# Performance work log

Hardware: AMD Instinct MI355X
Metric: run time of the kernel (lower is better)

## Reference

```python
import math
import jax, jax.numpy as jnp
import numpy as np

LMAX = 6
F_ACT = 16   # f_out // 8, channels through SO3Activation
F_MID = 64   # f_out // 2
N_A, N_B, N_C = 16, 8, 16  # SO(3) Euler-angle grid (resolution=8 quadrature in beta)
SQRT2 = math.sqrt(2.0)     # normalize2mom factor for relu

# ---- Wigner-D machinery (numpy, setup-time constants; mirrors e3nn conventions) ----

def _su2_generators(j):
    m = np.arange(-j, j)
    raising = np.diag(-np.sqrt(j * (j + 1) - m * (m + 1)), k=-1).astype(complex)
    m = np.arange(-j + 1, j + 1)
    lowering = np.diag(np.sqrt(j * (j + 1) - m * (m - 1)), k=1).astype(complex)
    m = np.arange(-j, j + 1)
    return np.stack([0.5 * (raising + lowering), np.diag(1j * m), -0.5j * (raising - lowering)])

def _q_real(l):
    q = np.zeros((2 * l + 1, 2 * l + 1), dtype=complex)
    for m in range(-l, 0):
        q[l + m, l + abs(m)] = 2 ** -0.5
        q[l + m, l - abs(m)] = -1j * 2 ** -0.5
    q[l, l] = 1
    for m in range(1, l + 1):
        q[l + m, l + abs(m)] = (-1) ** m * 2 ** -0.5
        q[l + m, l - abs(m)] = 1j * (-1) ** m * 2 ** -0.5
    return (-1j) ** l * q

def _so3_generators(l):
    X = _su2_generators(l)
    Q = _q_real(l)
    return np.real(np.einsum('ij,njk,kl->nil', np.conj(Q.T), X, Q))

def _expm(A):
    w, V = np.linalg.eig(A.astype(complex))
    return np.real((V * np.exp(w)) @ np.linalg.inv(V))

def _wigner_prod_grid(lmax, a, b, c):
    # flat_wigner on a product Euler grid: D(a,b,g) = exp(a*Jy) exp(b*Jx) exp(g*Jy)
    blocks = []
    for l in range(lmax + 1):
        X = _so3_generators(l)
        Ea = np.stack([_expm(t * X[1]) for t in a])
        Eb = np.stack([_expm(t * X[0]) for t in b])
        Ec = np.stack([_expm(t * X[1]) for t in c])
        D = np.einsum('amn,bnp,cpq->abcmq', Ea, Eb, Ec)
        blocks.append((2 * l + 1) ** 0.5 * D.reshape(len(a) * len(b) * len(c), -1))
    return np.concatenate(blocks, -1)

def _flat_wigner_pts(lmax, a, b, c):
    blocks = []
    for l in range(lmax + 1):
        X = _so3_generators(l)
        D = np.stack([_expm(ai * X[1]) @ _expm(bi * X[0]) @ _expm(ci * X[1]) for ai, bi, ci in zip(a, b, c)])
        blocks.append((2 * l + 1) ** 0.5 * D.reshape(len(a), -1))
    return np.concatenate(blocks, -1)

def _c8_angles():
    # escnn rot2dOnR2(8) elements, transposed and embedded into 3x3 with z fixed
    th = 2 * np.pi * np.arange(8) / 8
    M = np.zeros((8, 3, 3))
    M[:, 0, 0] = np.cos(th); M[:, 0, 1] = np.sin(th)
    M[:, 1, 0] = -np.sin(th); M[:, 1, 1] = np.cos(th)
    M[:, 2, 2] = 1.0
    x = M @ np.array([0.0, 1.0, 0.0])
    b = np.arccos(np.clip(x[:, 1], -1, 1))
    a = np.arctan2(x[:, 0], x[:, 2])
    def my(t): c, s = np.cos(t), np.sin(t); return np.array([[c, 0, s], [0, 1, 0], [-s, 0, c]])
    def mx(t): c, s = np.cos(t), np.sin(t); return np.array([[1, 0, 0], [0, c, -s], [0, s, c]])
    g = np.array([np.arctan2(R[0, 2], R[0, 0]) for R in [(my(a[i]) @ mx(b[i])).T @ M[i] for i in range(8)]])
    return a, b, g

# ---- precomputed constants ----
_A = 2 * np.pi * np.arange(N_A) / N_A
_XB, _WB = np.polynomial.legendre.leggauss(N_B)
_B = np.arccos(_XB)
_C = 2 * np.pi * np.arange(N_C) / N_C
D_IN = jnp.asarray(_wigner_prod_grid(1, _A, _B, _C), jnp.float32)                 # (G, 10)
_QW = np.broadcast_to((_WB / 2.0)[None, :, None] / (N_A * N_C), (N_A, N_B, N_C)).reshape(-1)
D_OUTW = jnp.asarray(_wigner_prod_grid(LMAX, _A, _B, _C) * _QW[:, None], jnp.float32)  # (G, 455), quadrature folded in
C8W = jnp.asarray(_flat_wigner_pts(LMAX, *_c8_angles()), jnp.float32)             # (8, 455)


def setup_inputs() -> dict:
    key = jax.random.key(0)
    ks = jax.random.split(key, 16)
    inp = {
        'x': jax.random.normal(ks[0], (16, 32, 128, 455), jnp.float32),
        'trajectory': jax.random.normal(ks[1], (16, 32, 10), jnp.float32),
        'w1_l0': jax.random.normal(ks[2], (1, F_ACT, 1, 1), jnp.float32),
        'w1_l1': jax.random.normal(ks[3], (1, F_ACT, 3, 3), jnp.float32),
    }
    for l in range(LMAX + 1):
        d = 2 * l + 1
        inp[f'w2_l{l}'] = jax.random.normal(ks[4 + l], (F_ACT, F_MID, d, d), jnp.float32)
    return inp


def reference(x, trajectory, w1_l0, w1_l1, w2_l0, w2_l1, w2_l2, w2_l3, w2_l4, w2_l5, w2_l6):
    w2s = [w2_l0, w2_l1, w2_l2, w2_l3, w2_l4, w2_l5, w2_l6]
    b, t, _ = trajectory.shape
    # pack trajectory into irreps 1x0e + 3x1e: scalar is last input component
    ti = jnp.concatenate([trajectory[..., 9:10], trajectory[..., :9]], axis=-1)  # (b,t,10)
    # proj_1 (o3.Linear, f_in=1 -> f_out=16), per-l block mixing with 1/sqrt(f_in*mul_in)
    o0 = ti[:, :, None, 0:1] * w1_l0[0, :, 0, 0][None, None, :, None]            # (b,t,16,1)
    x1 = ti[..., 1:10].reshape(b, t, 3, 3)                                       # (mul=3, m=3)
    o1 = jnp.einsum('btum,guw->btgwm', x1, w1_l1[0]) * (3.0 ** -0.5)             # (b,t,16,3,3)
    feat = jnp.concatenate([o0, o1.reshape(b, t, F_ACT, 9)], axis=-1)            # (b,t,16,10)
    # SO3Activation: irreps -> SO(3) grid -> relu (2nd-moment normalized) -> irreps up to LMAX
    sig = jnp.einsum('btci,gi->btcg', feat, D_IN)                                # (b,t,16,G)
    sig = jax.nn.relu(sig) * SQRT2
    feat = jnp.einsum('btcg,gi->btci', sig, D_OUTW)                              # (b,t,16,455)
    # proj_2 (o3.Linear on so3_irreps(6), f 16->64), block-diagonal per l
    outs = []
    off = 0
    for l in range(LMAX + 1):
        d = 2 * l + 1
        blk = feat[..., off:off + d * d].reshape(b, t, F_ACT, d, d)
        o = jnp.einsum('btfum,fguw->btgwm', blk, w2s[l]) * ((F_ACT * d) ** -0.5)
        outs.append(o.reshape(b, t, F_MID, d * d))
        off += d * d
    traj_out = jnp.concatenate(outs, axis=-1)                                    # (b,t,64,455)
    # Wigner-D projection onto C8 group elements
    traj_c8 = jnp.einsum('btcj,ij->btci', traj_out, C8W)                         # (b,t,64,8)
    x_c8 = jnp.einsum('bhcj,ij->bhci', x, C8W)                                   # (b,h,128,8)
    return x_c8, traj_c8
```

## Files before the change

kernel.cpp:

```cpp
#include <hip/hip_runtime.h>
#include <hip/hip_bf16.h>
#include <math.h>


typedef __attribute__((ext_vector_type(8))) short bf16x8;
typedef __attribute__((ext_vector_type(4))) float f32x4;
typedef __attribute__((ext_vector_type(16))) float f32x16;

__device__ const int c_offs[8] = {0, 1, 10, 35, 84, 165, 286, 455};

struct SetupArgs {
  double angA[16];
  double angB[8];
  double c8a[8], c8b[8], c8g[8];
};
struct QWArgs { double wb[8]; };
struct W2Ptrs { const void* p[7]; };

__device__ __forceinline__ float bf2f(unsigned short u) {
  union { unsigned int i; float f; } v; v.i = ((unsigned int)u) << 16; return v.f;
}
__device__ __forceinline__ unsigned short f2bf(float f) {
  union { float f; unsigned int i; } v; v.f = f;
  unsigned int r = v.i + 0x7fffu + ((v.i >> 16) & 1u);
  return (unsigned short)(r >> 16);
}
__device__ __forceinline__ float in_val(const void* p, size_t i, int isf) {
  return isf ? ((const float*)p)[i] : bf2f(((const unsigned short*)p)[i]);
}
__device__ __forceinline__ void gl_lds16(const void* g, void* lds) {
  __builtin_amdgcn_global_load_lds(
      (const __attribute__((address_space(1))) unsigned int*)g,
      (__attribute__((address_space(3))) unsigned int*)lds, 16, 0, 0);
}
__device__ __forceinline__ void wait_bar() {
  asm volatile("s_waitcnt vmcnt(0)\n\ts_barrier" ::: "memory");
}

__global__ __launch_bounds__(192) void k_exps(SetupArgs args, double* exps,
                                              const void* x, int* flag) {
  __shared__ double Qr[169], Qi[169], Bm[169], R[169];
  __shared__ double coefA[13], coefB[13], rowsum[13];
  __shared__ double snorm;
  __shared__ int cnt;
  int tid = threadIdx.x;

  if (blockIdx.x == 336) {
    if (tid == 0) cnt = 0;
    __syncthreads();
    if (tid < 64) {
      float v = ((const float*)x)[tid];
      float a = fabsf(v);
      int ok = (v == v) && (a > 9.0949470e-13f) && (a < 1.0995116e12f);
      atomicAdd(&cnt, ok);
    }
    __syncthreads();
    if (tid == 0) *flag = (cnt >= 32) ? 1 : 0;
    return;
  }

  int l = blockIdx.x / 48, item = blockIdx.x % 48;
  int e = tid;
  bool val = (e < 169);
  int r = e / 13, c = e % 13;

  if (val) { Qr[e] = 0.0; Qi[e] = 0.0; }
  __syncthreads();
  if (tid == 0) {
    const double is2 = 0.70710678118654752440;
    for (int m = -l; m <= l; m++) {
      int rr = l + m;
      if (m < 0) {
        Qr[rr * 13 + (l - m)] = is2;
        Qi[rr * 13 + (l + m)] = -is2;
      } else if (m == 0) {
        Qr[l * 13 + l] = 1.0;
      } else {
        double s = (m & 1) ? -1.0 : 1.0;
        Qr[rr * 13 + (l + m)] = s * is2;
        Qi[rr * 13 + (l - m)] = s * is2;
      }
    }
  }
  double jj = (double)l;
  if (tid < 13) {
    double m1 = (double)(tid - 1 - l);
    coefA[tid] = -0.5 * sqrt(fmax(jj * (jj + 1.0) - m1 * (m1 + 1.0), 0.0));
    double m2 = (double)(tid + 1 - l);
    coefB[tid] = 0.5 * sqrt(fmax(jj * (jj + 1.0) - m2 * (m2 - 1.0), 0.0));
  }
  __syncthreads();
  {
    int lm = l & 3;
    double pr = (lm == 0) ? 1.0 : (lm == 2 ? -1.0 : 0.0);
    double pi = (lm == 1) ? -1.0 : (lm == 3 ? 1.0 : 0.0);
    if (val) {
      double qr = Qr[e], qi = Qi[e];
      Qr[e] = qr * pr - qi * pi;
      Qi[e] = qr * pi + qi * pr;
    }
  }
  __syncthreads();

  double t; int axis;
  if (item < 16)      { t = args.angA[item];      axis = 1; }
  else if (item < 24) { t = args.angB[item - 16]; axis = 0; }
  else if (item < 32) { t = args.c8a[item - 24];  axis = 1; }
  else if (item < 40) { t = args.c8b[item - 32];  axis = 0; }
  else                { t = args.c8g[item - 40];  axis = 1; }

  if (val) {
    double accr = 0.0;
    if (axis == 1) {
#pragma unroll
      for (int p = 0; p < 13; p++) {
        double mp = (double)(p - l);
        double ar = Qr[p * 13 + r], ai = -Qi[p * 13 + r];
        double br = Qr[p * 13 + c], bi = Qi[p * 13 + c];
        accr += -mp * (ar * bi + ai * br);
      }
    } else {
#pragma unroll
      for (int p = 0; p < 13; p++) {
        double xr = 0.0, xi = 0.0;
        if (p > 0) {
          double v = coefA[p];
          xr += v * Qr[(p - 1) * 13 + c]; xi += v * Qi[(p - 1) * 13 + c];
        }
        if (p < 12) {
          double v = coefB[p];
          xr += v * Qr[(p + 1) * 13 + c]; xi += v * Qi[(p + 1) * 13 + c];
        }
        double ar = Qr[p * 13 + r], ai = -Qi[p * 13 + r];
        accr += ar * xr - ai * xi;
      }
    }
    Bm[e] = t * accr;
  }
  __syncthreads();
  if (tid < 13) {
    double s = 0.0;
#pragma unroll
    for (int cc = 0; cc < 13; cc++) s += fabs(Bm[tid * 13 + cc]);
    rowsum[tid] = s;
  }
  __syncthreads();
  if (tid == 0) {
    double mx = 0.0;
#pragma unroll
    for (int rr = 0; rr < 13; rr++) mx = fmax(mx, rowsum[rr]);
    int s = 0;
    while (mx > 0.5 && s < 48) { mx *= 0.5; s++; }
    snorm = (double)s;
  }
  __syncthreads();
  int sq = (int)snorm;
  double sc = 1.0;
  for (int i = 0; i < sq; i++) sc *= 0.5;
  if (val) {
    double b = Bm[e] * sc;
    Bm[e] = b;
    R[e] = b / 16.0 + ((r == c) ? 1.0 : 0.0);
  }
  __syncthreads();
  for (int k = 15; k >= 1; k--) {
    double acc = 0.0;
    if (val) {
#pragma unroll
      for (int p = 0; p < 13; p++) acc += Bm[r * 13 + p] * R[p * 13 + c];
    }
    __syncthreads();
    if (val) R[e] = acc / (double)k + ((r == c) ? 1.0 : 0.0);
    __syncthreads();
  }
  for (int i = 0; i < sq; i++) {
    double acc = 0.0;
    if (val) {
#pragma unroll
      for (int p = 0; p < 13; p++) acc += R[r * 13 + p] * R[p * 13 + c];
    }
    __syncthreads();
    if (val) R[e] = acc;
    __syncthreads();
  }
  double* out = exps + (size_t)blockIdx.x * 169;
  if (val) out[e] = R[e];
}

__global__ __launch_bounds__(192) void k_assemble(const double* exps, QWArgs qw,
                                                  unsigned short* dwt, float* dint,
                                                  float* c8w,
                                                  const void* traj, const void* w1l0,
                                                  const void* w1l1, float* feat,
                                                  const int* flag) {
  __shared__ double Ea[169], Eb[169], Ec[169], T1[169];
  int tid = threadIdx.x;
  int bx = blockIdx.x;

  if (bx >= 3640) {
    int isf = __builtin_amdgcn_readfirstlane(flag[0]);
    int idx = (bx - 3640) * 192 + tid;
    if (idx >= 512 * 160) return;
    int bt = idx / 160, rem = idx % 160;
    int c = rem / 10, i = rem % 10;
    float v;
    if (i == 0) {
      v = in_val(traj, bt * 10 + 9, isf) * in_val(w1l0, c, isf);
    } else {
      int ii = i - 1, w = ii / 3, m = ii % 3;
      float acc = 0.0f;
      for (int u = 0; u < 3; u++)
        acc += in_val(traj, bt * 10 + 3 * u + m, isf) *
               in_val(w1l1, c * 9 + u * 3 + w, isf);
      v = acc * 0.57735026918962576f;
    }
    feat[idx] = v;
    return;
  }

  int e = tid;
  bool valp = (e < 169);
  int r = e / 13, c = e % 13;

  if (bx >= 3584) {
    int idx = bx - 3584;
    int l = idx / 8, ci = idx % 8;
    int d = 2 * l + 1;
    const double* pa = exps + (size_t)(l * 48 + 24 + ci) * 169;
    const double* pb = exps + (size_t)(l * 48 + 32 + ci) * 169;
    const double* pc = exps + (size_t)(l * 48 + 40 + ci) * 169;
    if (valp) { Ea[e] = pa[e]; Eb[e] = pb[e]; Ec[e] = pc[e]; }
    __syncthreads();
    if (valp) {
      double acc = 0.0;
#pragma unroll
      for (int p = 0; p < 13; p++) acc += Ea[r * 13 + p] * Eb[p * 13 + c];
      T1[e] = acc;
    }
    __syncthreads();
    double scale = sqrt((double)(2 * l + 1));
    if (valp) {
      double acc = 0.0;
#pragma unroll
      for (int p = 0; p < 13; p++) acc += T1[r * 13 + p] * Ec[p * 13 + c];
      if (r < d && c < d)
        c8w[ci * 512 + c_offs[l] + r * d + c] = (float)(scale * acc);
    }
    if (l == 0) {
      for (int jz = 455 + tid; jz < 512; jz += 192)
        c8w[ci * 512 + jz] = 0.0f;
    }
    return;
  }

  int l = bx / 512, rem = bx % 512;
  int a = rem >> 5, b = (rem >> 2) & 7, cg = rem & 3;
  int d = 2 * l + 1;
  const double* pa = exps + (size_t)(l * 48 + a) * 169;
  const double* pb = exps + (size_t)(l * 48 + 16 + b) * 169;
  if (valp) { Ea[e] = pa[e]; Eb[e] = pb[e]; }
  __syncthreads();
  if (valp) {
    double acc = 0.0;
#pragma unroll
    for (int p = 0; p < 13; p++) acc += Ea[r * 13 + p] * Eb[p * 13 + c];
    T1[e] = acc;
  }
  double scale = sqrt((double)(2 * l + 1));
  double qwv = qw.wb[b] * (1.0 / 512.0);
  bool inblk = valp && (r < d) && (c < d);
  int j = inblk ? (c_offs[l] + r * d + c) : 0;
  const double* ctab = exps + (size_t)(l * 48) * 169;
  for (int cc = cg * 4; cc < cg * 4 + 4; cc++) {
    __syncthreads();
    if (valp) Ec[e] = ctab[(size_t)cc * 169 + e];
    __syncthreads();
    int g = a * 128 + b * 16 + cc;
    if (valp) {
      double acc = 0.0;
#pragma unroll
      for (int p = 0; p < 13; p++) acc += T1[r * 13 + p] * Ec[p * 13 + c];
      if (inblk) {
        dwt[(size_t)j * 2048 + g] = f2bf((float)(scale * acc * qwv));
        if (l == 1) dint[(size_t)(1 + r * 3 + c) * 2048 + g] = (float)(scale * acc);
        if (l == 0 && e == 0) dint[g] = (float)(scale * acc);
      }
    }
    if (l == 0) {
      for (int jz = 455 + tid; jz < 512; jz += 192)
        dwt[(size_t)jz * 2048 + g] = 0;
    }
  }
}

__global__ __launch_bounds__(256) void k_sig(const float* feat, const float* dint,
                                             unsigned short* sig) {
  int bi = blockIdx.x >> 3;
  int g = ((blockIdx.x & 7) << 8) + threadIdx.x;
  float din[10];
#pragma unroll
  for (int i = 0; i < 10; i++) din[i] = dint[(size_t)i * 2048 + g];
  const float* fr = feat + bi * 160;
  for (int cc = 0; cc < 16; cc++) {
    float acc = 0.0f;
#pragma unroll
    for (int i = 0; i < 10; i++) acc += fr[cc * 10 + i] * din[i];
    acc = fmaxf(acc, 0.0f) * 1.41421356237309505f;
    sig[(size_t)(bi * 16 + cc) * 2048 + g] = f2bf(acc);
  }
}

__global__ __launch_bounds__(256) void k_ebuild(W2Ptrs w2, const float* c8w,
                                                unsigned short* et, const int* flag) {
  int isf = __builtin_amdgcn_readfirstlane(flag[0]);
  int base = (blockIdx.x * 256 + threadIdx.x) * 4;
  int n = base >> 13;
  int rest = base & 8191;
  int f = rest >> 9, jj0 = rest & 511;
  int g = n >> 3, i = n & 7;
  unsigned short ov[4];
#pragma unroll
  for (int s = 0; s < 4; s++) {
    int jj = jj0 + s;
    if (jj >= 455) { ov[s] = 0; continue; }
    int l    = (jj >= 1) + (jj >= 10) + (jj >= 35) + (jj >= 84) +
               (jj >= 165) + (jj >= 286);
    int offs = jj >= 286 ? 286 : jj >= 165 ? 165 : jj >= 84 ? 84 :
               jj >= 35 ? 35 : jj >= 10 ? 10 : jj >= 1 ? 1 : 0;
    int mg   = jj >= 286 ? 20165 : jj >= 165 ? 23832 : jj >= 84 ? 29128 :
               jj >= 35 ? 37450 : jj >= 10 ? 52429 : jj >= 1 ? 87382 : 262144;
    int d = 2 * l + 1;
    int rloc = jj - offs;
    int u = (rloc * mg) >> 18;
    int m = rloc - u * d;
    const void* wp = w2.p[0];
    wp = (l >= 1) ? w2.p[1] : wp;
    wp = (l >= 2) ? w2.p[2] : wp;
    wp = (l >= 3) ? w2.p[3] : wp;
    wp = (l >= 4) ? w2.p[4] : wp;
    wp = (l >= 5) ? w2.p[5] : wp;
    wp = (l >= 6) ? w2.p[6] : wp;
    float acc = 0.0f;
    for (int w = 0; w < d; w++) {
      float wv = in_val(wp, ((size_t)(f * 64 + g) * d + u) * d + w, isf);
      acc += wv * c8w[i * 512 + offs + w * d + m];
    }
    acc *= rsqrtf((float)(16 * d));
    ov[s] = f2bf(acc);
  }
  *(ushort4*)&et[(size_t)n * 8192 + f * 512 + jj0] =
      make_ushort4(ov[0], ov[1], ov[2], ov[3]);
}

__global__ __launch_bounds__(256) void k_gemm2(const unsigned short* A,
                                               const unsigned short* B,
                                               unsigned short* C) {
  __shared__ __align__(16) unsigned short As[2][128 * 64];
  __shared__ __align__(16) unsigned short Bs[2][64 * 64];
  int tid = threadIdx.x;
  int lane = tid & 63, wid = tid >> 6;
  int xcd = blockIdx.x & 7, bi = blockIdx.x >> 3;
  int mt = xcd * 8 + (bi >> 3), nt = bi & 7;
  int m0 = mt * 128, n0 = nt * 64;
  int wm = wid >> 1, wn = wid & 1;
  f32x16 acc[2];
#pragma unroll
  for (int t = 0; t < 2; t++)
#pragma unroll
    for (int r = 0; r < 16; r++) acc[t][r] = 0.0f;

  int r0 = tid >> 3;
  int kcl = (tid & 7) ^ (r0 & 7);
  const unsigned short* Abase = A + (size_t)m0 * 2048;
  const unsigned short* Bbase = B + (size_t)n0 * 2048;
  int mrow = (lane & 31);
  int xr = lane & 7;
  int khalf = lane >> 5;

  auto STAGE = [&](int buf, int kt) {
    int k0 = kt * 64;
#pragma unroll
    for (int i = 0; i < 4; i++)
      gl_lds16(Abase + (size_t)(i * 32 + r0) * 2048 + k0 + kcl * 8,
               &As[buf][i * 2048 + wid * 512]);
#pragma unroll
    for (int i = 0; i < 2; i++)
      gl_lds16(Bbase + (size_t)(i * 32 + r0) * 2048 + k0 + kcl * 8,
               &Bs[buf][i * 2048 + wid * 512]);
  };

  STAGE(0, 0);
  wait_bar();
  int cur = 0;
  for (int kt = 0; kt < 32; kt++) {
    if (kt < 31) STAGE(cur ^ 1, kt + 1);
#pragma unroll
    for (int q = 0; q < 4; q++) {
      int qc = q * 2 + khalf;
      bf16x8 bv = *(const bf16x8*)&Bs[cur][(wn * 32 + mrow) * 64 + (qc ^ xr) * 8];
#pragma unroll
      for (int t = 0; t < 2; t++) {
        bf16x8 av = *(const bf16x8*)&As[cur][(wm * 64 + t * 32 + mrow) * 64 + (qc ^ xr) * 8];
        acc[t] = __builtin_amdgcn_mfma_f32_32x32x16_bf16(av, bv, acc[t], 0, 0, 0);
      }
    }
    if (kt < 31) { wait_bar(); cur ^= 1; }
  }
  int col = n0 + wn * 32 + (lane & 31);
#pragma unroll
  for (int t = 0; t < 2; t++)
#pragma unroll
    for (int r = 0; r < 16; r++) {
      int row = m0 + wm * 64 + t * 32 + (r & 3) + 8 * (r >> 2) + 4 * (lane >> 5);
      C[(size_t)row * 512 + col] = f2bf(acc[t][r]);
    }
}

__global__ __launch_bounds__(256) void k_gemm3(const unsigned short* A,
                                               const unsigned short* B, float* Cp) {
  __shared__ __align__(16) unsigned short As[2][64 * 32];
  __shared__ __align__(16) unsigned short Bs[2][128 * 32];
  int tid = threadIdx.x, lane = tid & 63, wid = tid >> 6;
  int mt = blockIdx.x >> 5, kc = (blockIdx.x >> 2) & 7, nt = blockIdx.x & 3;
  int m0 = mt * 64, n0 = nt * 128;
  int wm = wid >> 1, wn = wid & 1;
  f32x4 acc[2][4];
#pragma unroll
  for (int a = 0; a < 2; a++)
#pragma unroll
    for (int b = 0; b < 4; b++) acc[a][b] = (f32x4){0.f, 0.f, 0.f, 0.f};
  int ar = tid >> 2, ak = (tid & 3) * 8;
  const unsigned short* Abase = A + (size_t)m0 * 8192 + kc * 1024;
  const unsigned short* Bbase = B + (size_t)n0 * 8192 + kc * 1024;
  int row = lane & 15, kq = (lane >> 4) * 8;

  auto STAGE = [&](int buf, int kt) {
    int k0 = kt * 32;
    gl_lds16(Abase + (size_t)ar * 8192 + k0 + ak, &As[buf][wid * 512]);
    gl_lds16(Bbase + (size_t)ar * 8192 + k0 + ak, &Bs[buf][wid * 512]);
    gl_lds16(Bbase + (size_t)(ar + 64) * 8192 + k0 + ak, &Bs[buf][2048 + wid * 512]);
  };

  STAGE(0, 0);
  wait_bar();
  int cur = 0;
  for (int kt = 0; kt < 32; kt++) {
    if (kt < 31) STAGE(cur ^ 1, kt + 1);
    bf16x8 af[2], bfr[4];
#pragma unroll
    for (int im = 0; im < 2; im++)
      af[im] = *(const bf16x8*)&As[cur][(wm * 32 + im * 16 + row) * 32 + kq];
#pragma unroll
    for (int in = 0; in < 4; in++)
      bfr[in] = *(const bf16x8*)&Bs[cur][(wn * 64 + in * 16 + row) * 32 + kq];
#pragma unroll
    for (int im = 0; im < 2; im++)
#pragma unroll
      for (int in = 0; in < 4; in++)
        acc[im][in] = __builtin_amdgcn_mfma_f32_16x16x32_bf16(af[im], bfr[in],
                                                              acc[im][in], 0, 0, 0);
    if (kt < 31) { wait_bar(); cur ^= 1; }
  }
  int col = lane & 15, rq = (lane >> 4) * 4;
  float* out = Cp + (size_t)kc * 262144;
#pragma unroll
  for (int im = 0; im < 2; im++)
#pragma unroll
    for (int in = 0; in < 4; in++)
#pragma unroll
      for (int r = 0; r < 4; r++) {
        int rr = m0 + wm * 32 + im * 16 + rq + r;
        int cc = n0 + wn * 64 + in * 16 + col;
        out[(size_t)rr * 512 + cc] = acc[im][in][r];
      }
}

__global__ __launch_bounds__(256) void k_xc8r(const void* x, const float* c8w,
                                              const float* Cp, void* dout,
                                              const int* flag) {
  int tid = threadIdx.x, lane = tid & 63, wid = tid >> 6;
  int isf = __builtin_amdgcn_readfirstlane(flag[0]);

  if (blockIdx.x >= 2048) {
    int idx = (blockIdx.x - 2048) * 256 + tid;
    const float4* c = (const float4*)Cp;
    float s0 = 0.f, s1 = 0.f, s2 = 0.f, s3 = 0.f;
#pragma unroll
    for (int p = 0; p < 8; p++) {
      float4 v = c[idx + p * 65536];
      s0 += v.x; s1 += v.y; s2 += v.z; s3 += v.w;
    }
    size_t base = 524288 + (size_t)idx * 4;
    if (isf) {
      float4 o; o.x = s0; o.y = s1; o.z = s2; o.w = s3;
      *(float4*)((float*)dout + base) = o;
    } else {
      unsigned int p0 = (unsigned int)f2bf(s0) | ((unsigned int)f2bf(s1) << 16);
      unsigned int p1 = (unsigned int)f2bf(s2) | ((unsigned int)f2bf(s3) << 16);
      uint2 pk; pk.x = p0; pk.y = p1;
      *(uint2*)((unsigned short*)dout + base) = pk;
    }
    return;
  }

  int gw = blockIdx.x * 4 + wid;
  float cw[8][8];
#pragma unroll
  for (int t = 0; t < 8; t++)
#pragma unroll
    for (int i = 0; i < 8; i++)
      cw[t][i] = c8w[i * 512 + t * 64 + lane];
  const float* xf = (const float*)x;
  const unsigned short* xh = (const unsigned short*)x;
  for (int r = gw * 8; r < gw * 8 + 8; r++) {
    float acc[8];
#pragma unroll
    for (int i = 0; i < 8; i++) acc[i] = 0.0f;
    if (isf) {
      const float* xr = xf + (size_t)r * 455;
#pragma unroll
      for (int t = 0; t < 8; t++) {
        int j = t * 64 + lane;
        float xv = (j < 455) ? xr[j] : 0.0f;
#pragma unroll
        for (int i = 0; i < 8; i++) acc[i] += xv * cw[t][i];
      }
    } else {
      const unsigned short* xr = xh + (size_t)r * 455;
#pragma unroll
      for (int t = 0; t < 8; t++) {
        int j = t * 64 + lane;
        float xv = (j < 455) ? bf2f(xr[j]) : 0.0f;
#pragma unroll
        for (int i = 0; i < 8; i++) acc[i] += xv * cw[t][i];
      }
    }
#pragma unroll
    for (int off = 1; off <= 4; off <<= 1)
#pragma unroll
      for (int i = 0; i < 8; i++) acc[i] += __shfl_xor(acc[i], off);
    int lg = lane & 7;
    float v = acc[0];
    v = (lg == 1) ? acc[1] : v;
    v = (lg == 2) ? acc[2] : v;
    v = (lg == 3) ? acc[3] : v;
    v = (lg == 4) ? acc[4] : v;
    v = (lg == 5) ? acc[5] : v;
    v = (lg == 6) ? acc[6] : v;
    v = (lg == 7) ? acc[7] : v;
    v += __shfl_xor(v, 8);
    v += __shfl_xor(v, 16);
    v += __shfl_xor(v, 32);
    if (lane < 8) {
      if (isf) ((float*)dout)[(size_t)r * 8 + lane] = v;
      else     ((unsigned short*)dout)[(size_t)r * 8 + lane] = f2bf(v);
    }
  }
}

extern "C" void kernel_launch(void* const* d_in, const int* in_sizes, int n_in,
                              void* d_out, int out_size, void* d_ws, size_t ws_size,
                              hipStream_t stream) {
  const void* x    = d_in[0];
  const void* traj = d_in[1];
  const void* w1l0 = d_in[2];
  const void* w1l1 = d_in[3];
  W2Ptrs w2;
  for (int l = 0; l < 7; l++) w2.p[l] = d_in[4 + l];

  char* ws = (char*)d_ws;
  double* exps          = (double*)(ws + 0);
  float* dint           = (float*)(ws + 458752);
  float* c8w            = (float*)(ws + 540672);
  unsigned short* dwt   = (unsigned short*)(ws + 573440);
  float* feat           = (float*)(ws + 2670592);
  unsigned short* sig   = (unsigned short*)(ws + 2998272);
  unsigned short* f2    = (unsigned short*)(ws + 36552704);
  unsigned short* et    = (unsigned short*)(ws + 44941312);
  float* cp             = (float*)(ws + 53329920);
  int* flag             = (int*)(ws + 61718528);

  SetupArgs sa; QWArgs qa;
  for (int i = 0; i < 16; i++) sa.angA[i] = 2.0 * M_PI * (double)i / 16.0;
  static const double XB[8] = {
    -0.9602898564975363, -0.7966664774136267, -0.5255324099163290,
    -0.1834346424956498,  0.1834346424956498,  0.5255324099163290,
     0.7966664774136267,  0.9602898564975363};
  static const double WBv[8] = {
     0.1012285362903763, 0.2223810344533745, 0.3137066458778873,
     0.3626837833783620, 0.3626837833783620, 0.3137066458778873,
     0.2223810344533745, 0.1012285362903763};
  for (int i = 0; i < 8; i++) { sa.angB[i] = acos(XB[i]); qa.wb[i] = WBv[i]; }
  for (int i = 0; i < 8; i++) {
    double th = 2.0 * M_PI * (double)i / 8.0;
    double Mm[3][3] = {{cos(th), sin(th), 0.0},
                       {-sin(th), cos(th), 0.0},
                       {0.0, 0.0, 1.0}};
    double x0 = Mm[0][1], x1 = Mm[1][1], x2 = Mm[2][1];
    double bb = acos(fmax(-1.0, fmin(1.0, x1)));
    double aa = atan2(x0, x2);
    double ca_ = cos(aa), sa_ = sin(aa), cb_ = cos(bb), sb_ = sin(bb);
    double MY[3][3] = {{ca_, 0, sa_}, {0, 1, 0}, {-sa_, 0, ca_}};
    double MX[3][3] = {{1, 0, 0}, {0, cb_, -sb_}, {0, sb_, cb_}};
    double P1[3][3], Rr[3][3];
    for (int r = 0; r < 3; r++)
      for (int c = 0; c < 3; c++) {
        double s = 0.0;
        for (int k = 0; k < 3; k++) s += MY[r][k] * MX[k][c];
        P1[r][c] = s;
      }
    for (int r = 0; r < 3; r++)
      for (int c = 0; c < 3; c++) {
        double s = 0.0;
        for (int k = 0; k < 3; k++) s += P1[k][r] * Mm[k][c];
        Rr[r][c] = s;
      }
    double gg = atan2(Rr[0][2], Rr[0][0]);
    sa.c8a[i] = aa; sa.c8b[i] = bb; sa.c8g[i] = gg;
  }

  k_exps<<<337, 192, 0, stream>>>(sa, exps, x, flag);
  k_assemble<<<4067, 192, 0, stream>>>(exps, qa, dwt, dint, c8w,
                                       traj, w1l0, w1l1, feat, flag);
  k_sig<<<4096, 256, 0, stream>>>(feat, dint, sig);
  k_ebuild<<<4096, 256, 0, stream>>>(w2, c8w, et, flag);
  k_gemm2<<<512, 256, 0, stream>>>(sig, dwt, f2);
  k_gemm3<<<256, 256, 0, stream>>>(f2, et, cp);
  k_xc8r<<<2304, 256, 0, stream>>>(x, c8w, cp, d_out, flag);
}
```

Baseline: 328.2 us.

## Vectorize assemble stores, merge sig/ebuild kernels, triple-buffer both GEMMs

k_assemble now has each block handle all 16 gamma angles, so the dwt and dint writes become 16-byte vector stores instead of scattered 2-byte and 4-byte ones. The launch grid shrinks to match. k_sig and k_ebuild are merged into one k_post launch to remove a kernel launch. Both GEMMs move from double to triple buffering with partial vmcnt waits, so loads run two stages ahead. k_gemm3 also switches to 64x64 tiles with twice as many blocks, which adds parallelism but raises redundant A-tile reloads.

```diff
diff --git a/kernel.cpp b/kernel.cpp
--- a/kernel.cpp
+++ b/kernel.cpp
@@ -32,9 +32,6 @@
   __builtin_amdgcn_global_load_lds(
       (const __attribute__((address_space(1))) unsigned int*)g,
       (__attribute__((address_space(3))) unsigned int*)lds, 16, 0, 0);
-}
-__device__ __forceinline__ void wait_bar() {
-  asm volatile("s_waitcnt vmcnt(0)\n\ts_barrier" ::: "memory");
 }
 
 __global__ __launch_bounds__(192) void k_exps(SetupArgs args, double* exps,
@@ -197,9 +194,9 @@
   int tid = threadIdx.x;
   int bx = blockIdx.x;
 
-  if (bx >= 3640) {
+  if (bx >= 952) {
     int isf = __builtin_amdgcn_readfirstlane(flag[0]);
-    int idx = (bx - 3640) * 192 + tid;
+    int idx = (bx - 952) * 192 + tid;
     if (idx >= 512 * 160) return;
     int bt = idx / 160, rem = idx % 160;
     int c = rem / 10, i = rem % 10;
@@ -222,8 +219,8 @@
   bool valp = (e < 169);
   int r = e / 13, c = e % 13;
 
-  if (bx >= 3584) {
-    int idx = bx - 3584;
+  if (bx >= 896) {
+    int idx = bx - 896;
     int l = idx / 8, ci = idx % 8;
     int d = 2 * l + 1;
     const double* pa = exps + (size_t)(l * 48 + 24 + ci) * 169;
@@ -253,8 +250,8 @@
     return;
   }
 
-  int l = bx / 512, rem = bx % 512;
-  int a = rem >> 5, b = (rem >> 2) & 7, cg = rem & 3;
+  int l = bx >> 7, rem = bx & 127;
+  int a = rem >> 3, b = rem & 7;
   int d = 2 * l + 1;
   const double* pa = exps + (size_t)(l * 48 + a) * 169;
   const double* pb = exps + (size_t)(l * 48 + 16 + b) * 169;
@@ -270,50 +267,74 @@
   double qwv = qw.wb[b] * (1.0 / 512.0);
   bool inblk = valp && (r < d) && (c < d);
   int j = inblk ? (c_offs[l] + r * d + c) : 0;
+  int g0 = a * 128 + b * 16;
   const double* ctab = exps + (size_t)(l * 48) * 169;
-  for (int cc = cg * 4; cc < cg * 4 + 4; cc++) {
+  unsigned int ow[8];
+  float dv[16];
+#pragma unroll
+  for (int cc = 0; cc < 16; cc++) {
     __syncthreads();
     if (valp) Ec[e] = ctab[(size_t)cc * 169 + e];
     __syncthreads();
-    int g = a * 128 + b * 16 + cc;
+    double acc = 0.0;
     if (valp) {
-      double acc = 0.0;
 #pragma unroll
       for (int p = 0; p < 13; p++) acc += T1[r * 13 + p] * Ec[p * 13 + c];
-      if (inblk) {
-        dwt[(size_t)j * 2048 + g] = f2bf((float)(scale * acc * qwv));
-        if (l == 1) dint[(size_t)(1 + r * 3 + c) * 2048 + g] = (float)(scale * acc);
-        if (l == 0 && e == 0) dint[g] = (float)(scale * acc);
-      }
+    }
+    unsigned int hv = (unsigned int)f2bf((float)(scale * acc * qwv));
+    if ((cc & 1) == 0) ow[cc >> 1] = hv;
+    else               ow[cc >> 1] |= hv << 16;
+    dv[cc] = (float)(scale * acc);
+  }
+  if (inblk) {
+    unsigned short* wp = &dwt[(size_t)j * 2048 + g0];
+    *(uint4*)&wp[0] = make_uint4(ow[0], ow[1], ow[2], ow[3]);
+    *(uint4*)&wp[8] = make_uint4(ow[4], ow[5], ow[6], ow[7]);
+    if (l == 1) {
+      float* dp = &dint[(size_t)(1 + r * 3 + c) * 2048 + g0];
+      *(float4*)&dp[0]  = make_float4(dv[0],  dv[1],  dv[2],  dv[3]);
+      *(float4*)&dp[4]  = make_float4(dv[4],  dv[5],  dv[6],  dv[7]);
+      *(float4*)&dp[8]  = make_float4(dv[8],  dv[9],  dv[10], dv[11]);
+      *(float4*)&dp[12] = make_float4(dv[12], dv[13], dv[14], dv[15]);
     }
     if (l == 0) {
-      for (int jz = 455 + tid; jz < 512; jz += 192)
-        dwt[(size_t)jz * 2048 + g] = 0;
-    }
-  }
-}
-
-__global__ __launch_bounds__(256) void k_sig(const float* feat, const float* dint,
-                                             unsigned short* sig) {
-  int bi = blockIdx.x >> 3;
-  int g = ((blockIdx.x & 7) << 8) + threadIdx.x;
-  float din[10];
-#pragma unroll
-  for (int i = 0; i < 10; i++) din[i] = dint[(size_t)i * 2048 + g];
-  const float* fr = feat + bi * 160;
-  for (int cc = 0; cc < 16; cc++) {
-    float acc = 0.0f;
-#pragma unroll
-    for (int i = 0; i < 10; i++) acc += fr[cc * 10 + i] * din[i];
-    acc = fmaxf(acc, 0.0f) * 1.41421356237309505f;
-    sig[(size_t)(bi * 16 + cc) * 2048 + g] = f2bf(acc);
-  }
-}
-
-__global__ __launch_bounds__(256) void k_ebuild(W2Ptrs w2, const float* c8w,
-                                                unsigned short* et, const int* flag) {
+      float* dp = &dint[g0];
+      *(float4*)&dp[0]  = make_float4(dv[0],  dv[1],  dv[2],  dv[3]);
+      *(float4*)&dp[4]  = make_float4(dv[4],  dv[5],  dv[6],  dv[7]);
+      *(float4*)&dp[8]  = make_float4(dv[8],  dv[9],  dv[10], dv[11]);
+      *(float4*)&dp[12] = make_float4(dv[12], dv[13], dv[14], dv[15]);
+    }
+  }
+  if (l == 0 && tid < 57) {
+    unsigned short* zp = &dwt[(size_t)(455 + tid) * 2048 + g0];
+    *(uint4*)&zp[0] = make_uint4(0, 0, 0, 0);
+    *(uint4*)&zp[8] = make_uint4(0, 0, 0, 0);
+  }
+}
+
+__global__ __launch_bounds__(256) void k_post(const float* feat, const float* dint,
+                                              unsigned short* sig, W2Ptrs w2,
+                                              const float* c8w, unsigned short* et,
+                                              const int* flag) {
+  int bx = blockIdx.x;
+  if (bx < 4096) {
+    int bi = bx >> 3;
+    int g = ((bx & 7) << 8) + threadIdx.x;
+    float din[10];
+#pragma unroll
+    for (int i = 0; i < 10; i++) din[i] = dint[(size_t)i * 2048 + g];
+    const float* fr = feat + bi * 160;
+    for (int cc = 0; cc < 16; cc++) {
+      float acc = 0.0f;
+#pragma unroll
+      for (int i = 0; i < 10; i++) acc += fr[cc * 10 + i] * din[i];
+      acc = fmaxf(acc, 0.0f) * 1.41421356237309505f;
+      sig[(size_t)(bi * 16 + cc) * 2048 + g] = f2bf(acc);
+    }
+    return;
+  }
   int isf = __builtin_amdgcn_readfirstlane(flag[0]);
-  int base = (blockIdx.x * 256 + threadIdx.x) * 4;
+  int base = ((bx - 4096) * 256 + threadIdx.x) * 4;
   int n = base >> 13;
   int rest = base & 8191;
   int f = rest >> 9, jj0 = rest & 511;
@@ -355,8 +376,8 @@
 __global__ __launch_bounds__(256) void k_gemm2(const unsigned short* A,
                                                const unsigned short* B,
                                                unsigned short* C) {
-  __shared__ __align__(16) unsigned short As[2][128 * 64];
-  __shared__ __align__(16) unsigned short Bs[2][64 * 64];
+  __shared__ __align__(16) unsigned short As[3][128 * 64];
+  __shared__ __align__(16) unsigned short Bs[3][64 * 64];
   int tid = threadIdx.x;
   int lane = tid & 63, wid = tid >> 6;
   int xcd = blockIdx.x & 7, bi = blockIdx.x >> 3;
@@ -390,21 +411,27 @@
   };
 
   STAGE(0, 0);
-  wait_bar();
-  int cur = 0;
+  STAGE(1, 1);
+  int cb = 0;
   for (int kt = 0; kt < 32; kt++) {
-    if (kt < 31) STAGE(cur ^ 1, kt + 1);
+    if (kt < 31) asm volatile("s_waitcnt vmcnt(6)" ::: "memory");
+    else         asm volatile("s_waitcnt vmcnt(0)" ::: "memory");
+    __builtin_amdgcn_s_barrier();
+    __builtin_amdgcn_sched_barrier(0);
+    const unsigned short* Ab = As[cb];
+    const unsigned short* Bb = Bs[cb];
 #pragma unroll
     for (int q = 0; q < 4; q++) {
       int qc = q * 2 + khalf;
-      bf16x8 bv = *(const bf16x8*)&Bs[cur][(wn * 32 + mrow) * 64 + (qc ^ xr) * 8];
+      bf16x8 bv = *(const bf16x8*)&Bb[(wn * 32 + mrow) * 64 + (qc ^ xr) * 8];
 #pragma unroll
       for (int t = 0; t < 2; t++) {
-        bf16x8 av = *(const bf16x8*)&As[cur][(wm * 64 + t * 32 + mrow) * 64 + (qc ^ xr) * 8];
+        bf16x8 av = *(const bf16x8*)&Ab[(wm * 64 + t * 32 + mrow) * 64 + (qc ^ xr) * 8];
         acc[t] = __builtin_amdgcn_mfma_f32_32x32x16_bf16(av, bv, acc[t], 0, 0, 0);
       }
     }
-    if (kt < 31) { wait_bar(); cur ^= 1; }
+    if (kt < 30) STAGE(cb == 0 ? 2 : cb - 1, kt + 2);
+    cb = (cb == 2) ? 0 : cb + 1;
   }
   int col = n0 + wn * 32 + (lane & 31);
 #pragma unroll
@@ -418,17 +445,17 @@
 
 __global__ __launch_bounds__(256) void k_gemm3(const unsigned short* A,
                                                const unsigned short* B, float* Cp) {
-  __shared__ __align__(16) unsigned short As[2][64 * 32];
-  __shared__ __align__(16) unsigned short Bs[2][128 * 32];
+  __shared__ __align__(16) unsigned short As[3][64 * 32];
+  __shared__ __align__(16) unsigned short Bs[3][64 * 32];
   int tid = threadIdx.x, lane = tid & 63, wid = tid >> 6;
-  int mt = blockIdx.x >> 5, kc = (blockIdx.x >> 2) & 7, nt = blockIdx.x & 3;
-  int m0 = mt * 64, n0 = nt * 128;
+  int kc = blockIdx.x >> 6, mt = (blockIdx.x >> 3) & 7, nt = blockIdx.x & 7;
+  int m0 = mt * 64, n0 = nt * 64;
   int wm = wid >> 1, wn = wid & 1;
-  f32x4 acc[2][4];
+  f32x4 acc[2][2];
 #pragma unroll
   for (int a = 0; a < 2; a++)
 #pragma unroll
-    for (int b = 0; b < 4; b++) acc[a][b] = (f32x4){0.f, 0.f, 0.f, 0.f};
+    for (int b = 0; b < 2; b++) acc[a][b] = (f32x4){0.f, 0.f, 0.f, 0.f};
   int ar = tid >> 2, ak = (tid & 3) * 8;
   const unsigned short* Abase = A + (size_t)m0 * 8192 + kc * 1024;
   const unsigned short* Bbase = B + (size_t)n0 * 8192 + kc * 1024;
@@ -438,39 +465,42 @@
     int k0 = kt * 32;
     gl_lds16(Abase + (size_t)ar * 8192 + k0 + ak, &As[buf][wid * 512]);
     gl_lds16(Bbase + (size_t)ar * 8192 + k0 + ak, &Bs[buf][wid * 512]);
-    gl_lds16(Bbase + (size_t)(ar + 64) * 8192 + k0 + ak, &Bs[buf][2048 + wid * 512]);
   };
 
   STAGE(0, 0);
-  wait_bar();
-  int cur = 0;
+  STAGE(1, 1);
+  int cb = 0;
   for (int kt = 0; kt < 32; kt++) {
-    if (kt < 31) STAGE(cur ^ 1, kt + 1);
-    bf16x8 af[2], bfr[4];
+    if (kt < 31) asm volatile("s_waitcnt vmcnt(2)" ::: "memory");
+    else         asm volatile("s_waitcnt vmcnt(0)" ::: "memory");
+    __builtin_amdgcn_s_barrier();
+    __builtin_amdgcn_sched_barrier(0);
+    bf16x8 af[2], bfr[2];
 #pragma unroll
     for (int im = 0; im < 2; im++)
-      af[im] = *(const bf16x8*)&As[cur][(wm * 32 + im * 16 + row) * 32 + kq];
-#pragma unroll
-    for (int in = 0; in < 4; in++)
-      bfr[in] = *(const bf16x8*)&Bs[cur][(wn * 64 + in * 16 + row) * 32 + kq];
+      af[im] = *(const bf16x8*)&As[cb][(wm * 32 + im * 16 + row) * 32 + kq];
+#pragma unroll
+    for (int in = 0; in < 2; in++)
+      bfr[in] = *(const bf16x8*)&Bs[cb][(wn * 32 + in * 16 + row) * 32 + kq];
 #pragma unroll
     for (int im = 0; im < 2; im++)
 #pragma unroll
-      for (int in = 0; in < 4; in++)
+      for (int in = 0; in < 2; in++)
         acc[im][in] = __builtin_amdgcn_mfma_f32_16x16x32_bf16(af[im], bfr[in],
                                                               acc[im][in], 0, 0, 0);
-    if (kt < 31) { wait_bar(); cur ^= 1; }
+    if (kt < 30) STAGE(cb == 0 ? 2 : cb - 1, kt + 2);
+    cb = (cb == 2) ? 0 : cb + 1;
   }
   int col = lane & 15, rq = (lane >> 4) * 4;
   float* out = Cp + (size_t)kc * 262144;
 #pragma unroll
   for (int im = 0; im < 2; im++)
 #pragma unroll
-    for (int in = 0; in < 4; in++)
+    for (int in = 0; in < 2; in++)
 #pragma unroll
       for (int r = 0; r < 4; r++) {
         int rr = m0 + wm * 32 + im * 16 + rq + r;
-        int cc = n0 + wn * 64 + in * 16 + col;
+        int cc = n0 + wn * 32 + in * 16 + col;
         out[(size_t)rr * 512 + cc] = acc[im][in][r];
       }
 }
@@ -620,11 +650,10 @@
   }
 
   k_exps<<<337, 192, 0, stream>>>(sa, exps, x, flag);
-  k_assemble<<<4067, 192, 0, stream>>>(exps, qa, dwt, dint, c8w,
+  k_assemble<<<1379, 192, 0, stream>>>(exps, qa, dwt, dint, c8w,
                                        traj, w1l0, w1l1, feat, flag);
-  k_sig<<<4096, 256, 0, stream>>>(feat, dint, sig);
-  k_ebuild<<<4096, 256, 0, stream>>>(w2, c8w, et, flag);
+  k_post<<<8192, 256, 0, stream>>>(feat, dint, sig, w2, c8w, et, flag);
   k_gemm2<<<512, 256, 0, stream>>>(sig, dwt, f2);
-  k_gemm3<<<256, 256, 0, stream>>>(f2, et, cp);
+  k_gemm3<<<512, 256, 0, stream>>>(f2, et, cp);
   k_xc8r<<<2304, 256, 0, stream>>>(x, c8w, cp, d_out, flag);
 }
```

Result: no change. 327.8 us (-0.1%).
